# Kernel tuning notes

Measured on AMD Instinct MI355X. Metric: run time of the kernel, lower is better.

Reference implementation:

```python
import jax, jax.numpy as jnp
import numpy as np

B, E, H, NH, NB = 8192, 1024, 4096, 16, 2   # batch, latent, ffn hidden, heads, blocks
HD = E // NH                                 # head dim = 64
CH, CD = 64, 4                               # control horizon, control dim
EPS = 1e-5


def setup_inputs() -> dict:
    key = jax.random.key(0)
    ks = iter(jax.random.split(key, 24))

    def rn(shape, scale=0.02):
        return jax.random.normal(next(ks), shape, jnp.float32) * scale

    return dict(
        z_initial=jax.random.normal(next(ks), (B, E), jnp.float32),
        current_controls=jax.random.normal(next(ks), (B, CH, CD), jnp.float32),
        trajectory_error=jax.random.normal(next(ks), (B, 2), jnp.float32),
        ctrl_W=rn((CH * CD, E)), ctrl_b=jnp.zeros((E,), jnp.float32),
        err_W=rn((2, E)), err_b=jnp.zeros((E,), jnp.float32),
        # per-block (stacked over leading NB axis) attention params
        Wq=rn((NB, E, E)), Wk=rn((NB, E, E)), Wv=rn((NB, E, E)), Wo=rn((NB, E, E)),
        bq=jnp.zeros((NB, E), jnp.float32), bk=jnp.zeros((NB, E), jnp.float32),
        bv=jnp.zeros((NB, E), jnp.float32), bo=jnp.zeros((NB, E), jnp.float32),
        ln1_g=jnp.ones((NB, E), jnp.float32), ln1_b=jnp.zeros((NB, E), jnp.float32),
        W1=rn((NB, E, H)), b1=jnp.zeros((NB, H), jnp.float32),
        W2=rn((NB, H, E)), b2=jnp.zeros((NB, E), jnp.float32),
        ln2_g=jnp.ones((NB, E), jnp.float32), ln2_b=jnp.zeros((NB, E), jnp.float32),
        num_inner_cycles=3,
    )


def _layernorm(x, g, b):
    m = jnp.mean(x, axis=-1, keepdims=True)
    v = jnp.mean(jnp.square(x - m), axis=-1, keepdims=True)
    return (x - m) * jax.lax.rsqrt(v + EPS) * g + b


def reference(z_initial, current_controls, trajectory_error,
              ctrl_W, ctrl_b, err_W, err_b,
              Wq, Wk, Wv, Wo, bq, bk, bv, bo,
              ln1_g, ln1_b, W1, b1, W2, b2, ln2_g, ln2_b,
              num_inner_cycles):
    b = z_initial.shape[0]
    z = z_initial + current_controls.reshape(b, -1) @ ctrl_W + ctrl_b
    z = z + trajectory_error @ err_W + err_b

    scale = 1.0 / jnp.sqrt(jnp.asarray(HD, jnp.float32))

    def block(z, i):
        zc = z + z_initial                       # context injection
        # seq_len == 1 multi-head self-attention (softmax over single key == 1)
        q = (zc @ Wq[i] + bq[i]).reshape(b, NH, HD)
        k = (zc @ Wk[i] + bk[i]).reshape(b, NH, HD)
        v = (zc @ Wv[i] + bv[i]).reshape(b, NH, HD)
        scores = jnp.einsum('bhd,bhd->bh', q, k) * scale   # [B, NH], one key
        a = jax.nn.softmax(scores[..., None], axis=-1)[..., 0]  # == 1
        attn = (a[..., None] * v).reshape(b, E)
        attn_out = attn @ Wo[i] + bo[i]
        z1 = _layernorm(zc + attn_out, ln1_g[i], ln1_b[i])
        ffn = jax.nn.silu(z1 @ W1[i] + b1[i]) @ W2[i] + b2[i]
        return _layernorm(z1 + ffn, ln2_g[i], ln2_b[i])

    for _ in range(int(num_inner_cycles)):
        for i in range(NB):
            z = block(z, i)
    return z
```

## Files before the change

kernel.cpp:

```cpp
#include <hip/hip_runtime.h>

typedef unsigned short u16;
typedef __attribute__((ext_vector_type(4))) float f32x4;
typedef __attribute__((ext_vector_type(8))) __bf16 bf16x8;

__device__ __forceinline__ u16 f2bf(float f) {
  unsigned u = __float_as_uint(f);
  u += 0x7fffu + ((u >> 16) & 1u);
  return (u16)(u >> 16);
}
__device__ __forceinline__ float bf2f(u16 h) {
  return __uint_as_float((unsigned)h << 16);
}

__device__ __forceinline__ void g2l16(const void* g, void* l) {
  __builtin_amdgcn_global_load_lds(
      (const __attribute__((address_space(1))) void*)g,
      (__attribute__((address_space(3))) void*)l, 16, 0, 0);
}

template <int MODE, int N, int K>
__global__ __launch_bounds__(256)
void gemm_bt(const u16* __restrict__ A, const u16* __restrict__ Bt,
             float* __restrict__ Cf, u16* __restrict__ Cb,
             const float* __restrict__ bias)
{
  __shared__ u16 sA[128 * 64];
  __shared__ u16 sB[128 * 64];
  const int tid = threadIdx.x;
  const int lane = tid & 63;
  const int wave = tid >> 6;
  const int wm = wave >> 1;
  const int wn = wave & 1;
  const long long row0 = (long long)blockIdx.x * 128;
  const long long col0 = (long long)blockIdx.y * 128;
  const int lm = lane & 15;
  const int lq = lane >> 4;

  const u16* gA[4];
  const u16* gB[4];
#pragma unroll
  for (int it = 0; it < 4; ++it) {
    int c = it * 256 + tid;
    int r = c >> 3;
    int js = (c & 7) ^ (r & 7);
    gA[it] = A + (row0 + r) * K + js * 8;
    gB[it] = Bt + (col0 + r) * K + js * 8;
  }

  f32x4 acc[4][4] = {};

  for (int k0 = 0; k0 < K; k0 += 64) {
#pragma unroll
    for (int it = 0; it < 4; ++it) {
      int ub = (it * 256 + wave * 64) * 8;
      g2l16(gA[it] + k0, &sA[ub]);
      g2l16(gB[it] + k0, &sB[ub]);
    }
    __syncthreads();
#pragma unroll
    for (int s = 0; s < 2; ++s) {
      bf16x8 af[4], bfr[4];
#pragma unroll
      for (int t = 0; t < 4; ++t) {
        int ra = wm * 64 + t * 16 + lm;
        int ja = (s * 4 + lq) ^ (ra & 7);
        af[t] = *(const bf16x8*)&sA[ra * 64 + ja * 8];
        int rb = wn * 64 + t * 16 + lm;
        int jb = (s * 4 + lq) ^ (rb & 7);
        bfr[t] = *(const bf16x8*)&sB[rb * 64 + jb * 8];
      }
#pragma unroll
      for (int i = 0; i < 4; ++i)
#pragma unroll
        for (int j = 0; j < 4; ++j)
          acc[i][j] = __builtin_amdgcn_mfma_f32_16x16x32_bf16(af[i], bfr[j], acc[i][j], 0, 0, 0);
    }
    __syncthreads();
  }

  const int rb0 = lq * 4;
#pragma unroll
  for (int i = 0; i < 4; ++i) {
#pragma unroll
    for (int j = 0; j < 4; ++j) {
      long long grow = row0 + wm * 64 + i * 16 + rb0;
      long long gcol = col0 + wn * 64 + j * 16 + lm;
      float bcol = (MODE == 1) ? bias[gcol] : 0.f;
#pragma unroll
      for (int r = 0; r < 4; ++r) {
        long long idx = (grow + r) * N + gcol;
        float v = acc[i][j][r];
        if (MODE == 0) {
          Cf[idx] = v;
        } else if (MODE == 1) {
          float x = v + bcol;
          float sv = x / (1.f + __expf(-x));
          Cb[idx] = f2bf(sv);
        } else {
          Cb[idx] = f2bf(v);
        }
      }
    }
  }
}

__global__ __launch_bounds__(256)
void ln1_kernel(const u16* __restrict__ zc, const u16* __restrict__ Y,
                const float* __restrict__ bvo, const float* __restrict__ g,
                const float* __restrict__ b, u16* __restrict__ z1b)
{
  const int row = blockIdx.x * 4 + (threadIdx.x >> 6);
  const int lane = threadIdx.x & 63;
  const long long base = (long long)row * 1024;
  const ushort4* pz = (const ushort4*)(zc + base);
  const ushort4* py = (const ushort4*)(Y + base);
  const float4* pb = (const float4*)bvo;
  float4 x[4];
  float s = 0.f, s2 = 0.f;
#pragma unroll
  for (int i = 0; i < 4; ++i) {
    int idx = lane + 64 * i;
    ushort4 a = pz[idx]; ushort4 yu = py[idx]; float4 bv = pb[idx];
    float4 v;
    v.x = bf2f(a.x) + bf2f(yu.x) + bv.x; v.y = bf2f(a.y) + bf2f(yu.y) + bv.y;
    v.z = bf2f(a.z) + bf2f(yu.z) + bv.z; v.w = bf2f(a.w) + bf2f(yu.w) + bv.w;
    x[i] = v;
    s  += v.x + v.y + v.z + v.w;
    s2 += v.x * v.x + v.y * v.y + v.z * v.z + v.w * v.w;
  }
#pragma unroll
  for (int off = 32; off > 0; off >>= 1) {
    s  += __shfl_xor(s, off);
    s2 += __shfl_xor(s2, off);
  }
  const float mean = s * (1.0f / 1024.0f);
  const float var = s2 * (1.0f / 1024.0f) - mean * mean;
  const float rs = rsqrtf(var + 1e-5f);
  const float4* pg = (const float4*)g;
  const float4* pbb = (const float4*)b;
  ushort4* pob = (ushort4*)(z1b + base);
#pragma unroll
  for (int i = 0; i < 4; ++i) {
    int idx = lane + 64 * i;
    float4 gg = pg[idx], b2 = pbb[idx], v = x[i], o;
    o.x = (v.x - mean) * rs * gg.x + b2.x;
    o.y = (v.y - mean) * rs * gg.y + b2.y;
    o.z = (v.z - mean) * rs * gg.z + b2.z;
    o.w = (v.w - mean) * rs * gg.w + b2.w;
    pob[idx] = make_ushort4(f2bf(o.x), f2bf(o.y), f2bf(o.z), f2bf(o.w));
  }
}

__global__ __launch_bounds__(256)
void ln2_kernel(const u16* __restrict__ z1, const u16* __restrict__ F,
                const float* __restrict__ b2c, const float* __restrict__ g,
                const float* __restrict__ b, const float* __restrict__ zinit,
                float* __restrict__ zout, u16* __restrict__ zcb, int write_zc)
{
  const int row = blockIdx.x * 4 + (threadIdx.x >> 6);
  const int lane = threadIdx.x & 63;
  const long long base = (long long)row * 1024;
  const ushort4* pz = (const ushort4*)(z1 + base);
  const ushort4* pf = (const ushort4*)(F + base);
  const float4* pb = (const float4*)b2c;
  float4 x[4];
  float s = 0.f, s2 = 0.f;
#pragma unroll
  for (int i = 0; i < 4; ++i) {
    int idx = lane + 64 * i;
    ushort4 a = pz[idx]; ushort4 fu = pf[idx]; float4 bv = pb[idx];
    float4 v;
    v.x = bf2f(a.x) + bf2f(fu.x) + bv.x; v.y = bf2f(a.y) + bf2f(fu.y) + bv.y;
    v.z = bf2f(a.z) + bf2f(fu.z) + bv.z; v.w = bf2f(a.w) + bf2f(fu.w) + bv.w;
    x[i] = v;
    s  += v.x + v.y + v.z + v.w;
    s2 += v.x * v.x + v.y * v.y + v.z * v.z + v.w * v.w;
  }
#pragma unroll
  for (int off = 32; off > 0; off >>= 1) {
    s  += __shfl_xor(s, off);
    s2 += __shfl_xor(s2, off);
  }
  const float mean = s * (1.0f / 1024.0f);
  const float var = s2 * (1.0f / 1024.0f) - mean * mean;
  const float rs = rsqrtf(var + 1e-5f);
  const float4* pg = (const float4*)g;
  const float4* pbb = (const float4*)b;
  const float4* pzi = (const float4*)(zinit + base);
#pragma unroll
  for (int i = 0; i < 4; ++i) {
    int idx = lane + 64 * i;
    float4 gg = pg[idx], bb = pbb[idx], v = x[i], o;
    o.x = (v.x - mean) * rs * gg.x + bb.x;
    o.y = (v.y - mean) * rs * gg.y + bb.y;
    o.z = (v.z - mean) * rs * gg.z + bb.z;
    o.w = (v.w - mean) * rs * gg.w + bb.w;
    if (zout) ((float4*)(zout + base))[idx] = o;
    if (write_zc) {
      float4 zi = pzi[idx];
      ((ushort4*)(zcb + base))[idx] = make_ushort4(
          f2bf(o.x + zi.x), f2bf(o.y + zi.y), f2bf(o.z + zi.z), f2bf(o.w + zi.w));
    }
  }
}

__global__ __launch_bounds__(256)
void prologue_fin(const float* __restrict__ zinit, const u16* __restrict__ Yc,
                  const float* __restrict__ ctrl_b, const float* __restrict__ err,
                  const float* __restrict__ err_W, const float* __restrict__ err_b,
                  u16* __restrict__ zcb)
{
  const int row = blockIdx.x * 4 + (threadIdx.x >> 6);
  const int lane = threadIdx.x & 63;
  const long long base = (long long)row * 1024;
  const float e0 = err[row * 2 + 0];
  const float e1 = err[row * 2 + 1];
  const float4* pz = (const float4*)(zinit + base);
  const ushort4* py = (const ushort4*)(Yc + base);
  const float4* pcb = (const float4*)ctrl_b;
  const float4* pw0 = (const float4*)err_W;
  const float4* pw1 = (const float4*)(err_W + 1024);
  const float4* peb = (const float4*)err_b;
  ushort4* pzb = (ushort4*)(zcb + base);
#pragma unroll
  for (int i = 0; i < 4; ++i) {
    int idx = lane + 64 * i;
    float4 zi = pz[idx]; ushort4 yu = py[idx];
    float4 cb = pcb[idx], w0 = pw0[idx], w1 = pw1[idx], eb = peb[idx];
    pzb[idx] = make_ushort4(
        f2bf(zi.x + bf2f(yu.x) + cb.x + e0 * w0.x + e1 * w1.x + eb.x + zi.x),
        f2bf(zi.y + bf2f(yu.y) + cb.y + e0 * w0.y + e1 * w1.y + eb.y + zi.y),
        f2bf(zi.z + bf2f(yu.z) + cb.z + e0 * w0.z + e1 * w1.z + eb.z + zi.z),
        f2bf(zi.w + bf2f(yu.w) + cb.w + e0 * w0.w + e1 * w1.w + eb.w + zi.w));
  }
}

__global__ void transpose_cvt(const float* __restrict__ in, u16* __restrict__ out,
                              int R, int C)
{
  __shared__ float tile[32][33];
  const int x = blockIdx.x * 32 + threadIdx.x;
  const int y0 = blockIdx.y * 32;
#pragma unroll
  for (int i = 0; i < 32; i += 8)
    tile[threadIdx.y + i][threadIdx.x] = in[(long long)(y0 + threadIdx.y + i) * C + x];
  __syncthreads();
  const int ox = y0 + threadIdx.x;
  const int oy0 = blockIdx.x * 32;
#pragma unroll
  for (int i = 0; i < 32; i += 8)
    out[(long long)(oy0 + threadIdx.y + i) * R + ox] = f2bf(tile[threadIdx.x][threadIdx.y + i]);
}

__global__ void cvt_bf16(const float* __restrict__ in, u16* __restrict__ out, int n4)
{
  int i = blockIdx.x * 256 + threadIdx.x;
  if (i < n4) {
    float4 v = ((const float4*)in)[i];
    ((ushort4*)out)[i] = make_ushort4(f2bf(v.x), f2bf(v.y), f2bf(v.z), f2bf(v.w));
  }
}

__global__ void bias_fold(const float* __restrict__ bv, const float* __restrict__ Wo,
                          const float* __restrict__ bo, float* __restrict__ bvo)
{
  __shared__ float red[256];
  const int el = threadIdx.x & 63;
  const int e = blockIdx.x * 64 + el;
  const int q = threadIdx.x >> 6;
  float s = 0.f;
  for (int k = q * 256; k < q * 256 + 256; ++k) s += bv[k] * Wo[k * 1024 + e];
  red[threadIdx.x] = s;
  __syncthreads();
  if (q == 0) bvo[e] = red[el] + red[64 + el] + red[128 + el] + red[192 + el] + bo[e];
}

extern "C" void kernel_launch(void* const* d_in, const int* in_sizes, int n_in,
                              void* d_out, int out_size, void* d_ws, size_t ws_size,
                              hipStream_t stream)
{
  const float* z_init = (const float*)d_in[0];
  const float* ctrl   = (const float*)d_in[1];
  const float* err    = (const float*)d_in[2];
  const float* ctrl_W = (const float*)d_in[3];
  const float* ctrl_b = (const float*)d_in[4];
  const float* err_W  = (const float*)d_in[5];
  const float* err_b  = (const float*)d_in[6];
  const float* Wv    = (const float*)d_in[9];
  const float* Wo    = (const float*)d_in[10];
  const float* bv    = (const float*)d_in[13];
  const float* bo    = (const float*)d_in[14];
  const float* ln1_g = (const float*)d_in[15];
  const float* ln1_b = (const float*)d_in[16];
  const float* W1    = (const float*)d_in[17];
  const float* b1    = (const float*)d_in[18];
  const float* W2    = (const float*)d_in[19];
  const float* b2    = (const float*)d_in[20];
  const float* ln2_g = (const float*)d_in[21];
  const float* ln2_b = (const float*)d_in[22];

  constexpr int B = 8192, E = 1024, H = 4096;

  char* p = (char*)d_ws;
  auto alloc = [&](size_t bytes) {
    char* r = p;
    p += (bytes + 255) & ~(size_t)255;
    return r;
  };
  u16*   tmp_b  = (u16*)alloc((size_t)B * E * 2);
  u16*   zc_b   = (u16*)alloc((size_t)B * E * 2);
  u16*   z1_b   = (u16*)alloc((size_t)B * E * 2);
  u16*   h_b    = (u16*)alloc((size_t)B * H * 2);
  u16*   ctrl16 = (u16*)alloc((size_t)B * 256 * 2);
  u16*   ctrlWT = (u16*)alloc((size_t)E * 256 * 2);
  u16*   Wv16   = (u16*)alloc((size_t)2 * E * E * 2);
  u16*   WoT    = (u16*)alloc((size_t)2 * E * E * 2);
  u16*   WvoT   = (u16*)alloc((size_t)2 * E * E * 2);
  u16*   W1T    = (u16*)alloc((size_t)2 * E * H * 2);
  u16*   W2T    = (u16*)alloc((size_t)2 * E * H * 2);
  float* bvo    = (float*)alloc((size_t)2 * E * 4);

  dim3 blk256(256);
  dim3 blkT(32, 8);

  cvt_bf16<<<(B * 256 / 4 + 255) / 256, blk256, 0, stream>>>(ctrl, ctrl16, B * 256 / 4);
  transpose_cvt<<<dim3(E / 32, 256 / 32), blkT, 0, stream>>>(ctrl_W, ctrlWT, 256, E);
  for (int i = 0; i < 2; ++i) {
    cvt_bf16<<<(E * E / 4 + 255) / 256, blk256, 0, stream>>>(Wv + (size_t)i * E * E, Wv16 + (size_t)i * E * E, E * E / 4);
    transpose_cvt<<<dim3(E / 32, E / 32), blkT, 0, stream>>>(Wo + (size_t)i * E * E, WoT + (size_t)i * E * E, E, E);
    transpose_cvt<<<dim3(H / 32, E / 32), blkT, 0, stream>>>(W1 + (size_t)i * E * H, W1T + (size_t)i * E * H, E, H);
    transpose_cvt<<<dim3(E / 32, H / 32), blkT, 0, stream>>>(W2 + (size_t)i * E * H, W2T + (size_t)i * E * H, H, E);
    bias_fold<<<E / 64, blk256, 0, stream>>>(bv + i * E, Wo + (size_t)i * E * E, bo + i * E, bvo + i * E);
  }
  for (int i = 0; i < 2; ++i)
    gemm_bt<2, E, E><<<dim3(E / 128, E / 128), blk256, 0, stream>>>(
        WoT + (size_t)i * E * E, Wv16 + (size_t)i * E * E,
        nullptr, WvoT + (size_t)i * E * E, nullptr);

  gemm_bt<2, E, 256><<<dim3(B / 128, E / 128), blk256, 0, stream>>>(
      ctrl16, ctrlWT, nullptr, tmp_b, nullptr);
  prologue_fin<<<B / 4, blk256, 0, stream>>>(z_init, tmp_b, ctrl_b, err, err_W, err_b, zc_b);

  for (int it = 0; it < 6; ++it) {
    int i = it & 1;
    int last = (it == 5);
    gemm_bt<2, E, E><<<dim3(B / 128, E / 128), blk256, 0, stream>>>(
        zc_b, WvoT + (size_t)i * E * E, nullptr, tmp_b, nullptr);
    ln1_kernel<<<B / 4, blk256, 0, stream>>>(zc_b, tmp_b, bvo + i * E,
        ln1_g + (size_t)i * E, ln1_b + (size_t)i * E, z1_b);
    gemm_bt<1, H, E><<<dim3(B / 128, H / 128), blk256, 0, stream>>>(
        z1_b, W1T + (size_t)i * E * H, nullptr, h_b, b1 + (size_t)i * H);
    gemm_bt<2, E, H><<<dim3(B / 128, E / 128), blk256, 0, stream>>>(
        h_b, W2T + (size_t)i * E * H, nullptr, tmp_b, nullptr);
    ln2_kernel<<<B / 4, blk256, 0, stream>>>(z1_b, tmp_b, b2 + (size_t)i * E,
        ln2_g + (size_t)i * E, ln2_b + (size_t)i * E, z_init,
        last ? (float*)d_out : nullptr, zc_b, last ? 0 : 1);
  }
}
```

Before: 1.610 ms.

## Add 256x256 pipelined MFMA GEMM with split-K for the FFN matmuls

Adds a new 512-thread GEMM kernel that uses 256x256 output tiles, swizzled LDS staged with direct global-to-LDS loads, double buffering with interleaved MFMA phases, and a grid remap across the eight XCDs. The two FFN GEMMs (W1 with fused SiLU, and W2) now use it. W2 uses split-K by two, writing two partial bf16 outputs that ln2_kernel adds together. The larger tiles and deeper pipelining aim to raise MFMA utilisation and reuse. In exchange the code carries more register and LDS pressure, an extra partial buffer to read and write, and some extra rounding from the bf16 partial sums.

```diff
diff --git a/kernel.cpp b/kernel.cpp
--- a/kernel.cpp
+++ b/kernel.cpp
@@ -17,6 +17,234 @@
   __builtin_amdgcn_global_load_lds(
       (const __attribute__((address_space(1))) void*)g,
       (__attribute__((address_space(3))) void*)l, 16, 0, 0);
+}
+
+#define BAR() __builtin_amdgcn_s_barrier()
+#define SCHED0() __builtin_amdgcn_sched_barrier(0)
+#define LGKM0()                                         \
+  do {                                                  \
+    asm volatile("s_waitcnt lgkmcnt(0)" ::: "memory");  \
+    SCHED0();                                           \
+  } while (0)
+#define VMCNT(n)                                          \
+  do {                                                    \
+    asm volatile("s_waitcnt vmcnt(" #n ")" ::: "memory"); \
+  } while (0)
+
+template <int MODE, int SPLIT, int NBN, int K>
+__global__ __launch_bounds__(512, 2)
+void gemm256(const u16* __restrict__ A, const u16* __restrict__ Bt,
+             u16* __restrict__ Cb, const float* __restrict__ bias)
+{
+  constexpr int N = NBN * 256;
+  constexpr int LDA = SPLIT * K;
+  constexpr int LDB = SPLIT * K;
+  constexpr int NT = K / 64;
+  constexpr int NITER = NT / 2;
+  static_assert(NITER >= 2, "pipeline needs >= 4 K-tiles");
+
+  __shared__ __align__(16) u16 lds[2][4][8192];
+
+  const int tid = threadIdx.x;
+  const int lane = tid & 63;
+  const int wave = tid >> 6;
+  const int wm = wave >> 2;
+  const int wn = wave & 3;
+  const int lm = lane & 15;
+  const int lq = lane >> 4;
+  const int swz = lm & 7;
+  const int j0 = lq ^ swz;
+  const int j1 = (4 + lq) ^ swz;
+
+  const int nwg = (int)gridDim.x;
+  const int bid = (int)blockIdx.x;
+  const int id = (bid & 7) * (nwg >> 3) + (bid >> 3);
+  const int bps = (SPLIT == 1) ? nwg : (nwg / SPLIT);
+  const int sp = (SPLIT == 1) ? 0 : (id / bps);
+  const int rres = (SPLIT == 1) ? id : (id % bps);
+  const int bm = rres / NBN;
+  const int bn = rres % NBN;
+  const long long row0 = (long long)bm * 256;
+  const long long col0 = (long long)bn * 256;
+  const int M = (bps / NBN) * 256;
+  const long long spK = (long long)sp * K;
+
+  const int rh = tid >> 3;
+  const int jj = tid & 7;
+  const u16* gA[2];
+  const u16* gB[2];
+  {
+    const int jsA = jj ^ (rh & 7);
+#pragma unroll
+    for (int h = 0; h < 2; ++h)
+      gA[h] = A + (row0 + h * 64 + rh) * LDA + spK + jsA * 8;
+    const int st = rh >> 5, c32 = rh & 31;
+    const int jsB = jj ^ (c32 & 7);
+#pragma unroll
+    for (int h = 0; h < 2; ++h)
+      gB[h] = Bt + (col0 + st * 64 + h * 32 + c32) * LDB + spK + jsB * 8;
+  }
+  const int ldsBase0 = wave * 64 * 8;
+
+  auto stageA = [&](int buf, int h, int tk) {
+    const u16* s = gA[h] + tk * 64;
+    g2l16(s, &lds[buf][h][ldsBase0]);
+    g2l16(s + 128 * LDA, &lds[buf][h][ldsBase0 + 4096]);
+  };
+  auto stageB = [&](int buf, int h, int tk) {
+    const u16* s = gB[h] + tk * 64;
+    g2l16(s, &lds[buf][2 + h][ldsBase0]);
+    g2l16(s + 128 * LDB, &lds[buf][2 + h][ldsBase0 + 4096]);
+  };
+
+  bf16x8 fa[4][2], fbA[2][2], fbB[2][2];
+  auto loadFA = [&](int buf, int h) {
+    const u16* u = &lds[buf][h][0];
+#pragma unroll
+    for (int t = 0; t < 4; ++t) {
+      const u16* rp = u + (wm * 64 + t * 16 + lm) * 64;
+      fa[t][0] = *(const bf16x8*)(rp + j0 * 8);
+      fa[t][1] = *(const bf16x8*)(rp + j1 * 8);
+    }
+  };
+  auto loadFB = [&](bf16x8 (*dst)[2], int buf, int h) {
+    const u16* u = &lds[buf][2 + h][0];
+#pragma unroll
+    for (int c = 0; c < 2; ++c) {
+      const u16* rp = u + (wn * 32 + c * 16 + lm) * 64;
+      dst[c][0] = *(const bf16x8*)(rp + j0 * 8);
+      dst[c][1] = *(const bf16x8*)(rp + j1 * 8);
+    }
+  };
+
+  f32x4 acc[8][4] = {};
+
+#define QMFMA(RB, CB, FB)                                                   \
+  do {                                                                      \
+    __builtin_amdgcn_s_setprio(1);                                          \
+    _Pragma("unroll") for (int r_ = 0; r_ < 4; ++r_) {                      \
+      _Pragma("unroll") for (int c_ = 0; c_ < 2; ++c_) {                    \
+        acc[RB + r_][CB + c_] = __builtin_amdgcn_mfma_f32_16x16x32_bf16(    \
+            fa[r_][0], FB[c_][0], acc[RB + r_][CB + c_], 0, 0, 0);          \
+        acc[RB + r_][CB + c_] = __builtin_amdgcn_mfma_f32_16x16x32_bf16(    \
+            fa[r_][1], FB[c_][1], acc[RB + r_][CB + c_], 0, 0, 0);          \
+      }                                                                     \
+    }                                                                       \
+    __builtin_amdgcn_s_setprio(0);                                          \
+  } while (0)
+
+  stageA(0, 0, 0); stageA(0, 1, 0); stageB(0, 0, 0); stageB(0, 1, 0);
+  stageA(1, 0, 1); stageB(1, 1, 1);
+  VMCNT(4);
+  BAR();
+
+#pragma unroll 1
+  for (int i = 0; i < NITER - 1; ++i) {
+    const int tk = 2 * i;
+    loadFA(0, 0); loadFB(fbA, 0, 0);
+    stageA(1, 1, tk + 1);
+    BAR(); LGKM0();
+    QMFMA(0, 0, fbA);
+    BAR();
+    loadFB(fbB, 0, 1);
+    stageB(1, 0, tk + 1);
+    BAR(); LGKM0();
+    QMFMA(0, 2, fbB);
+    BAR();
+    loadFA(0, 1);
+    stageA(0, 0, tk + 2);
+    BAR(); LGKM0();
+    QMFMA(4, 2, fbB);
+    BAR();
+    stageB(0, 1, tk + 2);
+    VMCNT(4);
+    BAR();
+    QMFMA(4, 0, fbA);
+    BAR();
+    loadFA(1, 0); loadFB(fbA, 1, 0);
+    stageA(0, 1, tk + 2);
+    BAR(); LGKM0();
+    QMFMA(0, 0, fbA);
+    BAR();
+    loadFB(fbB, 1, 1);
+    stageB(0, 0, tk + 2);
+    BAR(); LGKM0();
+    QMFMA(0, 2, fbB);
+    BAR();
+    loadFA(1, 1);
+    stageA(1, 0, tk + 3);
+    BAR(); LGKM0();
+    QMFMA(4, 2, fbB);
+    BAR();
+    stageB(1, 1, tk + 3);
+    VMCNT(4);
+    BAR();
+    QMFMA(4, 0, fbA);
+    BAR();
+  }
+  {
+    const int tk = 2 * (NITER - 1);
+    loadFA(0, 0); loadFB(fbA, 0, 0);
+    stageA(1, 1, tk + 1);
+    BAR(); LGKM0();
+    QMFMA(0, 0, fbA);
+    BAR();
+    loadFB(fbB, 0, 1);
+    stageB(1, 0, tk + 1);
+    BAR(); LGKM0();
+    QMFMA(0, 2, fbB);
+    BAR();
+    loadFA(0, 1);
+    BAR(); LGKM0();
+    QMFMA(4, 2, fbB);
+    BAR();
+    VMCNT(0);
+    BAR();
+    QMFMA(4, 0, fbA);
+    BAR();
+    loadFA(1, 0); loadFB(fbA, 1, 0);
+    BAR(); LGKM0();
+    QMFMA(0, 0, fbA);
+    BAR();
+    loadFB(fbB, 1, 1);
+    BAR(); LGKM0();
+    QMFMA(0, 2, fbB);
+    BAR();
+    loadFA(1, 1);
+    BAR(); LGKM0();
+    QMFMA(4, 2, fbB);
+    BAR();
+    QMFMA(4, 0, fbA);
+  }
+#undef QMFMA
+
+  u16* Cout = Cb + (size_t)sp * ((size_t)M * N);
+  float bcol[4];
+  if (MODE == 1) {
+#pragma unroll
+    for (int cb = 0; cb < 4; ++cb)
+      bcol[cb] = bias[col0 + wn * 64 + cb * 16 + lm];
+  }
+#pragma unroll
+  for (int rb = 0; rb < 8; ++rb) {
+    const long long grow = row0 + wm * 128 + rb * 16 + lq * 4;
+#pragma unroll
+    for (int cb = 0; cb < 4; ++cb) {
+      const long long gcol = col0 + wn * 64 + cb * 16 + lm;
+#pragma unroll
+      for (int r = 0; r < 4; ++r) {
+        long long idx = (grow + r) * N + gcol;
+        float v = acc[rb][cb][r];
+        if (MODE == 1) {
+          float x = v + bcol[cb];
+          Cout[idx] = f2bf(x / (1.f + __expf(-x)));
+        } else {
+          Cout[idx] = f2bf(v);
+        }
+      }
+    }
+  }
+  (void)bias;
 }
 
 template <int MODE, int N, int K>
@@ -154,25 +382,30 @@
 
 __global__ __launch_bounds__(256)
 void ln2_kernel(const u16* __restrict__ z1, const u16* __restrict__ F,
-                const float* __restrict__ b2c, const float* __restrict__ g,
-                const float* __restrict__ b, const float* __restrict__ zinit,
-                float* __restrict__ zout, u16* __restrict__ zcb, int write_zc)
+                const u16* __restrict__ F2, const float* __restrict__ b2c,
+                const float* __restrict__ g, const float* __restrict__ b,
+                const float* __restrict__ zinit, float* __restrict__ zout,
+                u16* __restrict__ zcb, int write_zc)
 {
   const int row = blockIdx.x * 4 + (threadIdx.x >> 6);
   const int lane = threadIdx.x & 63;
   const long long base = (long long)row * 1024;
   const ushort4* pz = (const ushort4*)(z1 + base);
   const ushort4* pf = (const ushort4*)(F + base);
+  const ushort4* pf2 = (const ushort4*)(F2 + base);
   const float4* pb = (const float4*)b2c;
   float4 x[4];
   float s = 0.f, s2 = 0.f;
 #pragma unroll
   for (int i = 0; i < 4; ++i) {
     int idx = lane + 64 * i;
-    ushort4 a = pz[idx]; ushort4 fu = pf[idx]; float4 bv = pb[idx];
+    ushort4 a = pz[idx]; ushort4 fu = pf[idx]; ushort4 f2u = pf2[idx];
+    float4 bv = pb[idx];
     float4 v;
-    v.x = bf2f(a.x) + bf2f(fu.x) + bv.x; v.y = bf2f(a.y) + bf2f(fu.y) + bv.y;
-    v.z = bf2f(a.z) + bf2f(fu.z) + bv.z; v.w = bf2f(a.w) + bf2f(fu.w) + bv.w;
+    v.x = bf2f(a.x) + bf2f(fu.x) + bf2f(f2u.x) + bv.x;
+    v.y = bf2f(a.y) + bf2f(fu.y) + bf2f(f2u.y) + bv.y;
+    v.z = bf2f(a.z) + bf2f(fu.z) + bf2f(f2u.z) + bv.z;
+    v.w = bf2f(a.w) + bf2f(fu.w) + bf2f(f2u.w) + bv.w;
     x[i] = v;
     s  += v.x + v.y + v.z + v.w;
     s2 += v.x * v.x + v.y * v.y + v.z * v.z + v.w * v.w;
@@ -308,7 +541,8 @@
     p += (bytes + 255) & ~(size_t)255;
     return r;
   };
-  u16*   tmp_b  = (u16*)alloc((size_t)B * E * 2);
+  u16*   tmp_b  = (u16*)alloc((size_t)2 * B * E * 2);
+  u16*   tmp2_b = tmp_b + (size_t)B * E;
   u16*   zc_b   = (u16*)alloc((size_t)B * E * 2);
   u16*   z1_b   = (u16*)alloc((size_t)B * E * 2);
   u16*   h_b    = (u16*)alloc((size_t)B * H * 2);
@@ -322,6 +556,7 @@
   float* bvo    = (float*)alloc((size_t)2 * E * 4);
 
   dim3 blk256(256);
+  dim3 blk512(512);
   dim3 blkT(32, 8);
 
   cvt_bf16<<<(B * 256 / 4 + 255) / 256, blk256, 0, stream>>>(ctrl, ctrl16, B * 256 / 4);
@@ -349,11 +584,11 @@
         zc_b, WvoT + (size_t)i * E * E, nullptr, tmp_b, nullptr);
     ln1_kernel<<<B / 4, blk256, 0, stream>>>(zc_b, tmp_b, bvo + i * E,
         ln1_g + (size_t)i * E, ln1_b + (size_t)i * E, z1_b);
-    gemm_bt<1, H, E><<<dim3(B / 128, H / 128), blk256, 0, stream>>>(
-        z1_b, W1T + (size_t)i * E * H, nullptr, h_b, b1 + (size_t)i * H);
-    gemm_bt<2, E, H><<<dim3(B / 128, E / 128), blk256, 0, stream>>>(
-        h_b, W2T + (size_t)i * E * H, nullptr, tmp_b, nullptr);
-    ln2_kernel<<<B / 4, blk256, 0, stream>>>(z1_b, tmp_b, b2 + (size_t)i * E,
+    gemm256<1, 1, H / 256, E><<<dim3((B / 256) * (H / 256)), blk512, 0, stream>>>(
+        z1_b, W1T + (size_t)i * E * H, h_b, b1 + (size_t)i * H);
+    gemm256<2, 2, E / 256, H / 2><<<dim3((B / 256) * (E / 256) * 2), blk512, 0, stream>>>(
+        h_b, W2T + (size_t)i * E * H, tmp_b, nullptr);
+    ln2_kernel<<<B / 4, blk256, 0, stream>>>(z1_b, tmp_b, tmp2_b, b2 + (size_t)i * E,
         ln2_g + (size_t)i * E, ln2_b + (size_t)i * E, z_init,
         last ? (float*)d_out : nullptr, zc_b, last ? 0 : 1);
   }
```

Measured after the change: 1.470 ms. -8.7%, faster.

## Add 256x128 double-buffered GEMM with split-K and fold partials into LayerNorm

Applied to the files above, without the earlier changes.

Introduces a new 512-thread GEMM kernel with 256x128 tiles, double-buffered LDS staging via direct global-to-LDS loads, XOR-swizzled LDS layout, XCD-aware block remapping and MFMA priority hints. The two E-output GEMMs use 2-way split-K to raise the block count, and the two bf16 partial outputs are summed inside the LayerNorm kernels. The goal is better MFMA utilisation and occupancy on the main GEMMs. The cost is extra partial-buffer memory traffic, plus an added bf16 rounding of each partial sum.

```diff
diff --git a/kernel.cpp b/kernel.cpp
--- a/kernel.cpp
+++ b/kernel.cpp
@@ -17,6 +17,142 @@
   __builtin_amdgcn_global_load_lds(
       (const __attribute__((address_space(1))) void*)g,
       (__attribute__((address_space(3))) void*)l, 16, 0, 0);
+}
+
+#define BAR() __builtin_amdgcn_s_barrier()
+#define VMCNT(n)                                          \
+  do {                                                    \
+    asm volatile("s_waitcnt vmcnt(" #n ")" ::: "memory"); \
+  } while (0)
+
+template <int MODE, int SPLIT, int NBN, int K>
+__global__ __launch_bounds__(512, 4)
+void gemm_v5(const u16* __restrict__ A, const u16* __restrict__ Bt,
+             u16* __restrict__ Cb, const float* __restrict__ bias)
+{
+  constexpr int N = NBN * 128;
+  constexpr int LDA = SPLIT * K;
+  constexpr int LDB = SPLIT * K;
+  constexpr int NT = K / 32;
+  static_assert(NT >= 2, "need >= 2 K-tiles");
+
+  __shared__ __align__(16) u16 lds[2 * 12288];
+
+  const int tid = threadIdx.x;
+  const int lane = tid & 63;
+  const int wave = tid >> 6;
+  const int wr = wave >> 1;
+  const int wc = wave & 1;
+  const int lm = lane & 15;
+  const int lq = lane >> 4;
+
+  const int nwg = (int)gridDim.x;
+  const int bid = (int)blockIdx.x;
+  const int id = (bid & 7) * (nwg >> 3) + (bid >> 3);
+  const int bps = (SPLIT == 1) ? nwg : (nwg / SPLIT);
+  const int sp = (SPLIT == 1) ? 0 : (id / bps);
+  const int rres = (SPLIT == 1) ? id : (id % bps);
+  const int bm = rres / NBN;
+  const int bn = rres % NBN;
+  const long long row0 = (long long)bm * 256;
+  const long long col0 = (long long)bn * 128;
+  const int M = (bps / NBN) * 256;
+  const long long spK = (long long)sp * K;
+
+  const int rh = tid >> 2;
+  const int jj = tid & 3;
+  const int js = jj ^ ((rh >> 1) & 3);
+  const u16* pA0 = A + (row0 + rh) * LDA + spK + js * 8;
+  const u16* pA1 = pA0 + 128 * LDA;
+  const u16* pB  = Bt + (col0 + rh) * LDB + spK + js * 8;
+
+  const int wb = wave * 512;
+
+  auto stage = [&](int buf) {
+    u16* d = lds + buf * 12288 + wb;
+    g2l16(pA0, d);
+    g2l16(pA1, d + 4096);
+    g2l16(pB,  d + 8192);
+    pA0 += 32; pA1 += 32; pB += 32;
+  };
+
+  bf16x8 fa[4], fb[4];
+  auto loadFrags = [&](int buf) {
+    const u16* uA = lds + buf * 12288;
+    const u16* uB = uA + 8192;
+#pragma unroll
+    for (int c = 0; c < 4; ++c) {
+      int col = wc * 64 + c * 16 + lm;
+      int sl = lq ^ ((col >> 1) & 3);
+      fb[c] = *(const bf16x8*)(uB + col * 32 + sl * 8);
+    }
+#pragma unroll
+    for (int t = 0; t < 4; ++t) {
+      int r = wr * 64 + t * 16 + lm;
+      int sl = lq ^ ((r >> 1) & 3);
+      fa[t] = *(const bf16x8*)(uA + r * 32 + sl * 8);
+    }
+  };
+
+  f32x4 acc[4][4] = {};
+
+  stage(0);
+
+#pragma unroll 1
+  for (int t = 0; t < NT - 1; ++t) {
+    stage((t + 1) & 1);
+    VMCNT(3);
+    BAR();
+    loadFrags(t & 1);
+    __builtin_amdgcn_s_setprio(1);
+#pragma unroll
+    for (int rb = 0; rb < 4; ++rb)
+#pragma unroll
+      for (int cb = 0; cb < 4; ++cb)
+        acc[rb][cb] = __builtin_amdgcn_mfma_f32_16x16x32_bf16(
+            fa[rb], fb[cb], acc[rb][cb], 0, 0, 0);
+    __builtin_amdgcn_s_setprio(0);
+    BAR();
+  }
+  VMCNT(0);
+  BAR();
+  loadFrags((NT - 1) & 1);
+  __builtin_amdgcn_s_setprio(1);
+#pragma unroll
+  for (int rb = 0; rb < 4; ++rb)
+#pragma unroll
+    for (int cb = 0; cb < 4; ++cb)
+      acc[rb][cb] = __builtin_amdgcn_mfma_f32_16x16x32_bf16(
+          fa[rb], fb[cb], acc[rb][cb], 0, 0, 0);
+  __builtin_amdgcn_s_setprio(0);
+
+  u16* Cout = Cb + (size_t)sp * ((size_t)M * N);
+  float bcol[4];
+  if (MODE == 1) {
+#pragma unroll
+    for (int cb = 0; cb < 4; ++cb)
+      bcol[cb] = bias[col0 + wc * 64 + cb * 16 + lm];
+  }
+#pragma unroll
+  for (int rb = 0; rb < 4; ++rb) {
+    const long long grow = row0 + wr * 64 + rb * 16 + lq * 4;
+#pragma unroll
+    for (int cb = 0; cb < 4; ++cb) {
+      const long long gcol = col0 + wc * 64 + cb * 16 + lm;
+#pragma unroll
+      for (int r = 0; r < 4; ++r) {
+        long long idx = (grow + r) * N + gcol;
+        float v = acc[rb][cb][r];
+        if (MODE == 1) {
+          float x = v + bcol[cb];
+          Cout[idx] = f2bf(x / (1.f + __expf(-x)));
+        } else {
+          Cout[idx] = f2bf(v);
+        }
+      }
+    }
+  }
+  (void)bias;
 }
 
 template <int MODE, int N, int K>
@@ -107,24 +243,29 @@
 
 __global__ __launch_bounds__(256)
 void ln1_kernel(const u16* __restrict__ zc, const u16* __restrict__ Y,
-                const float* __restrict__ bvo, const float* __restrict__ g,
-                const float* __restrict__ b, u16* __restrict__ z1b)
+                const u16* __restrict__ Y2, const float* __restrict__ bvo,
+                const float* __restrict__ g, const float* __restrict__ b,
+                u16* __restrict__ z1b)
 {
   const int row = blockIdx.x * 4 + (threadIdx.x >> 6);
   const int lane = threadIdx.x & 63;
   const long long base = (long long)row * 1024;
   const ushort4* pz = (const ushort4*)(zc + base);
   const ushort4* py = (const ushort4*)(Y + base);
+  const ushort4* py2 = (const ushort4*)(Y2 + base);
   const float4* pb = (const float4*)bvo;
   float4 x[4];
   float s = 0.f, s2 = 0.f;
 #pragma unroll
   for (int i = 0; i < 4; ++i) {
     int idx = lane + 64 * i;
-    ushort4 a = pz[idx]; ushort4 yu = py[idx]; float4 bv = pb[idx];
+    ushort4 a = pz[idx]; ushort4 yu = py[idx]; ushort4 y2 = py2[idx];
+    float4 bv = pb[idx];
     float4 v;
-    v.x = bf2f(a.x) + bf2f(yu.x) + bv.x; v.y = bf2f(a.y) + bf2f(yu.y) + bv.y;
-    v.z = bf2f(a.z) + bf2f(yu.z) + bv.z; v.w = bf2f(a.w) + bf2f(yu.w) + bv.w;
+    v.x = bf2f(a.x) + bf2f(yu.x) + bf2f(y2.x) + bv.x;
+    v.y = bf2f(a.y) + bf2f(yu.y) + bf2f(y2.y) + bv.y;
+    v.z = bf2f(a.z) + bf2f(yu.z) + bf2f(y2.z) + bv.z;
+    v.w = bf2f(a.w) + bf2f(yu.w) + bf2f(y2.w) + bv.w;
     x[i] = v;
     s  += v.x + v.y + v.z + v.w;
     s2 += v.x * v.x + v.y * v.y + v.z * v.z + v.w * v.w;
@@ -154,25 +295,30 @@
 
 __global__ __launch_bounds__(256)
 void ln2_kernel(const u16* __restrict__ z1, const u16* __restrict__ F,
-                const float* __restrict__ b2c, const float* __restrict__ g,
-                const float* __restrict__ b, const float* __restrict__ zinit,
-                float* __restrict__ zout, u16* __restrict__ zcb, int write_zc)
+                const u16* __restrict__ F2, const float* __restrict__ b2c,
+                const float* __restrict__ g, const float* __restrict__ b,
+                const float* __restrict__ zinit, float* __restrict__ zout,
+                u16* __restrict__ zcb, int write_zc)
 {
   const int row = blockIdx.x * 4 + (threadIdx.x >> 6);
   const int lane = threadIdx.x & 63;
   const long long base = (long long)row * 1024;
   const ushort4* pz = (const ushort4*)(z1 + base);
   const ushort4* pf = (const ushort4*)(F + base);
+  const ushort4* pf2 = (const ushort4*)(F2 + base);
   const float4* pb = (const float4*)b2c;
   float4 x[4];
   float s = 0.f, s2 = 0.f;
 #pragma unroll
   for (int i = 0; i < 4; ++i) {
     int idx = lane + 64 * i;
-    ushort4 a = pz[idx]; ushort4 fu = pf[idx]; float4 bv = pb[idx];
+    ushort4 a = pz[idx]; ushort4 fu = pf[idx]; ushort4 f2u = pf2[idx];
+    float4 bv = pb[idx];
     float4 v;
-    v.x = bf2f(a.x) + bf2f(fu.x) + bv.x; v.y = bf2f(a.y) + bf2f(fu.y) + bv.y;
-    v.z = bf2f(a.z) + bf2f(fu.z) + bv.z; v.w = bf2f(a.w) + bf2f(fu.w) + bv.w;
+    v.x = bf2f(a.x) + bf2f(fu.x) + bf2f(f2u.x) + bv.x;
+    v.y = bf2f(a.y) + bf2f(fu.y) + bf2f(f2u.y) + bv.y;
+    v.z = bf2f(a.z) + bf2f(fu.z) + bf2f(f2u.z) + bv.z;
+    v.w = bf2f(a.w) + bf2f(fu.w) + bf2f(f2u.w) + bv.w;
     x[i] = v;
     s  += v.x + v.y + v.z + v.w;
     s2 += v.x * v.x + v.y * v.y + v.z * v.z + v.w * v.w;
@@ -308,7 +454,8 @@
     p += (bytes + 255) & ~(size_t)255;
     return r;
   };
-  u16*   tmp_b  = (u16*)alloc((size_t)B * E * 2);
+  u16*   tmp_b  = (u16*)alloc((size_t)2 * B * E * 2);
+  u16*   tmp2_b = tmp_b + (size_t)B * E;
   u16*   zc_b   = (u16*)alloc((size_t)B * E * 2);
   u16*   z1_b   = (u16*)alloc((size_t)B * E * 2);
   u16*   h_b    = (u16*)alloc((size_t)B * H * 2);
@@ -322,6 +469,7 @@
   float* bvo    = (float*)alloc((size_t)2 * E * 4);
 
   dim3 blk256(256);
+  dim3 blk512(512);
   dim3 blkT(32, 8);
 
   cvt_bf16<<<(B * 256 / 4 + 255) / 256, blk256, 0, stream>>>(ctrl, ctrl16, B * 256 / 4);
@@ -345,15 +493,15 @@
   for (int it = 0; it < 6; ++it) {
     int i = it & 1;
     int last = (it == 5);
-    gemm_bt<2, E, E><<<dim3(B / 128, E / 128), blk256, 0, stream>>>(
-        zc_b, WvoT + (size_t)i * E * E, nullptr, tmp_b, nullptr);
-    ln1_kernel<<<B / 4, blk256, 0, stream>>>(zc_b, tmp_b, bvo + i * E,
+    gemm_v5<2, 2, E / 128, E / 2><<<dim3((B / 256) * (E / 128) * 2), blk512, 0, stream>>>(
+        zc_b, WvoT + (size_t)i * E * E, tmp_b, nullptr);
+    ln1_kernel<<<B / 4, blk256, 0, stream>>>(zc_b, tmp_b, tmp2_b, bvo + i * E,
         ln1_g + (size_t)i * E, ln1_b + (size_t)i * E, z1_b);
-    gemm_bt<1, H, E><<<dim3(B / 128, H / 128), blk256, 0, stream>>>(
-        z1_b, W1T + (size_t)i * E * H, nullptr, h_b, b1 + (size_t)i * H);
-    gemm_bt<2, E, H><<<dim3(B / 128, E / 128), blk256, 0, stream>>>(
-        h_b, W2T + (size_t)i * E * H, nullptr, tmp_b, nullptr);
-    ln2_kernel<<<B / 4, blk256, 0, stream>>>(z1_b, tmp_b, b2 + (size_t)i * E,
+    gemm_v5<1, 1, H / 128, E><<<dim3((B / 256) * (H / 128)), blk512, 0, stream>>>(
+        z1_b, W1T + (size_t)i * E * H, h_b, b1 + (size_t)i * H);
+    gemm_v5<2, 2, E / 128, H / 2><<<dim3((B / 256) * (E / 128) * 2), blk512, 0, stream>>>(
+        h_b, W2T + (size_t)i * E * H, tmp_b, nullptr);
+    ln2_kernel<<<B / 4, blk256, 0, stream>>>(z1_b, tmp_b, tmp2_b, b2 + (size_t)i * E,
         ln2_g + (size_t)i * E, ln2_b + (size_t)i * E, z_init,
         last ? (float*)d_out : nullptr, zc_b, last ? 0 : 1);
   }
```

Result: no change. 1.612 ms (+0.1%).
